# Kernel tuning notes

Measured on AMD Instinct MI355X. Metric: run time of the kernel, lower is better.

The kernel has to match this reference:

```python
import jax, jax.numpy as jnp
import numpy as np

W_SCALE = 0.1  # brevitas SignedBinaryWeightPerTensorConst default scaling_init
A_SCALE = 1.0  # brevitas SignedBinaryActPerTensorConst default scaling


def bin_weight(w):
    # fake-quant binary weight: scale * sign(w), STE identity gradient
    q = W_SCALE * jnp.sign(w)
    return w + jax.lax.stop_gradient(q - w)


def bin_act(x):
    # QuantHardTanh with signed binary act: clamp to [-1,1] then binarize (STE)
    y = jnp.clip(x, -A_SCALE, A_SCALE)
    q = A_SCALE * jnp.sign(y)
    return y + jax.lax.stop_gradient(q - y)


def conv1d(x, w, b, stride=1):
    # x: [N,C,L], w: [O,I,K]
    y = jax.lax.conv_general_dilated(x, w, (stride,), 'VALID',
                                     dimension_numbers=('NCH', 'OIH', 'NCH'))
    return y + b[None, :, None]


def maxpool4(x):
    return jax.lax.reduce_window(x, -jnp.inf, jax.lax.max,
                                 (1, 1, 4), (1, 1, 4), 'VALID')


def bn1d(x, s, o):
    # eval-mode BatchNorm folded to per-channel affine: scale s, bias o
    if x.ndim == 3:
        return x * s[None, :, None] + o[None, :, None]
    return x * s[None, :] + o[None, :]


def setup_inputs() -> dict:
    key = jax.random.key(0)
    ks = jax.random.split(key, 24)
    f = jax.random.normal
    inp = {
        'x': f(ks[0], (128, 1, 16000), jnp.float32),
        'w1': f(ks[1], (128, 1, 80), jnp.float32),
        'b1': f(ks[2], (128,), jnp.float32),
        'bn1_s': jax.random.uniform(ks[3], (128,), jnp.float32),
        'bn1_b': f(ks[4], (128,), jnp.float32),
        'w2': f(ks[5], (128, 128, 3), jnp.float32),
        'b2': f(ks[6], (128,), jnp.float32),
        'bn2_s': jax.random.uniform(ks[7], (128,), jnp.float32),
        'bn2_b': f(ks[8], (128,), jnp.float32),
        'w3': f(ks[9], (256, 128, 3), jnp.float32),
        'b3': f(ks[10], (256,), jnp.float32),
        'bn3_s': jax.random.uniform(ks[11], (256,), jnp.float32),
        'bn3_b': f(ks[12], (256,), jnp.float32),
        'w5': f(ks[13], (512, 256, 3), jnp.float32),
        'b5': f(ks[14], (512,), jnp.float32),
        'bn5_s': jax.random.uniform(ks[15], (512,), jnp.float32),
        'bn5_b': f(ks[16], (512,), jnp.float32),
        'w_emb': f(ks[17], (512, 512, 14), jnp.float32),
        'b_emb': f(ks[18], (512,), jnp.float32),
        'wfc1': f(ks[19], (256, 512), jnp.float32),
        'bnfc1_s': jax.random.uniform(ks[20], (256,), jnp.float32),
        'bnfc1_b': f(ks[21], (256,), jnp.float32),
        'wfc2': f(ks[22], (35, 256), jnp.float32),
    }
    return inp


def reference(x, w1, b1, bn1_s, bn1_b, w2, b2, bn2_s, bn2_b,
              w3, b3, bn3_s, bn3_b, w5, b5, bn5_s, bn5_b,
              w_emb, b_emb, wfc1, bnfc1_s, bnfc1_b, wfc2):
    x = conv1d(x, bin_weight(w1), b1, stride=4)      # [N,128,3981]
    x = maxpool4(bin_act(bn1d(x, bn1_s, bn1_b)))     # [N,128,995]
    x = conv1d(x, bin_weight(w2), b2)                # [N,128,993]
    x = maxpool4(bin_act(bn1d(x, bn2_s, bn2_b)))     # [N,128,248]
    x = conv1d(x, bin_weight(w3), b3)                # [N,256,246]
    x = maxpool4(bin_act(bn1d(x, bn3_s, bn3_b)))     # [N,256,61]
    x = conv1d(x, bin_weight(w5), b5)                # [N,512,59]
    x = maxpool4(bin_act(bn1d(x, bn5_s, bn5_b)))     # [N,512,14]
    x = conv1d(x, bin_weight(w_emb), b_emb)          # [N,512,1]
    x = x[:, :, 0]                                   # squeeze -> [N,512]
    x = x @ bin_weight(wfc1).T                       # [N,256]
    x = bin_act(bn1d(x, bnfc1_s, bnfc1_b))
    x = x @ bin_weight(wfc2).T                       # [N,35]
    return x
```

## Files before the change

### kernel.cpp

```cpp
#include <hip/hip_runtime.h>
#include <stdint.h>

__device__ __forceinline__ float dance(float w) {
  float q = w > 0.f ? 0.1f : (w < 0.f ? -0.1f : 0.0f);
  float r = __fsub_rn(q, w);
  return __fadd_rn(w, r);
}

__device__ __forceinline__ int sgn(float u) {
  return u > 0.f ? 1 : (u < 0.f ? -1 : 0);
}

__global__ void pack_dance_T(const float* __restrict__ w, float* __restrict__ out,
                             int OC, int K) {
  int idx = blockIdx.x * 256 + threadIdx.x;
  if (idx >= OC * K) return;
  int oc = idx / K, k = idx - oc * K;
  out[(size_t)k * OC + oc] = dance(w[idx]);
}

__global__ void pack_dance_W12(const float* __restrict__ w, float* __restrict__ out,
                               int OC, int K) {
  int idx = blockIdx.x * 256 + threadIdx.x;
  if (idx >= OC * K) return;
  int oc = idx / K, k = idx - oc * K;
  out[((size_t)(k / 12) * OC + oc) * 12 + (k % 12)] = dance(w[idx]);
}

__global__ void pack_dance_E4(const float* __restrict__ w, float* __restrict__ out,
                              int OC, int K) {
  int idx = blockIdx.x * 256 + threadIdx.x;
  if (idx >= OC * K) return;
  int r = idx >> 2;
  int lo = idx & 3;
  int oc = r % OC;
  int k4 = r / OC;
  out[idx] = dance(w[(size_t)oc * K + k4 * 4 + lo]);
}

__global__ __launch_bounds__(128) void conv1_fast(
    const float* __restrict__ x, const float* __restrict__ w1t,
    const float* __restrict__ b1, const float* __restrict__ s1,
    const float* __restrict__ o1, int8_t* __restrict__ a1) {
  const int tid = threadIdx.x;
  const int tp0 = blockIdx.x * 2;
  const int b0 = blockIdx.y * 2;
  float wreg[80];
#pragma unroll
  for (int k = 0; k < 80; ++k) wreg[k] = w1t[k * 128 + tid];

  const int sb0 = 4 * (min(tp0 + 0, 994) - tp0);
  const int sb1 = 4 * (min(tp0 + 1, 994) - tp0);
  const float4* xb0 = (const float4*)(x + (size_t)(b0 + 0) * 16000 + 16 * tp0);
  const float4* xb1 = (const float4*)(x + (size_t)(b0 + 1) * 16000 + 16 * tp0);
  float z[2][2][4] = {};
#pragma unroll
  for (int q = 0; q < 20; ++q) {
#pragma unroll
    for (int nb = 0; nb < 2; ++nb) {
      const float4* x4 = nb ? xb1 : xb0;
#pragma unroll
      for (int p = 0; p < 2; ++p) {
        const int sb = p ? sb1 : sb0;
        float4 v0 = x4[sb + q + 0];
        float4 v1 = x4[sb + q + 1];
        float4 v2 = x4[sb + q + 2];
        float4 v3 = x4[sb + q + 3];
        float4 vv[4] = {v0, v1, v2, v3};
#pragma unroll
        for (int g = 0; g < 4; ++g) {
          float zz = z[nb][p][g];
          zz = __builtin_fmaf(wreg[4 * q + 0], vv[g].x, zz);
          zz = __builtin_fmaf(wreg[4 * q + 1], vv[g].y, zz);
          zz = __builtin_fmaf(wreg[4 * q + 2], vv[g].z, zz);
          zz = __builtin_fmaf(wreg[4 * q + 3], vv[g].w, zz);
          z[nb][p][g] = zz;
        }
      }
    }
  }
  const float bv = b1[tid], sv = s1[tid], ov = o1[tid];
#pragma unroll
  for (int nb = 0; nb < 2; ++nb)
#pragma unroll
    for (int p = 0; p < 2; ++p) {
      int m = -2;
#pragma unroll
      for (int g = 0; g < 4; ++g) {
        float y = __fadd_rn(z[nb][p][g], bv);
        float t2 = __fmul_rn(y, sv);
        float u = __fadd_rn(t2, ov);
        m = max(m, sgn(u));
      }
      int tpc = min(tp0 + p, 994);
      a1[((size_t)(b0 + nb) * 995 + tpc) * 128 + tid] = (int8_t)m;
    }
}

template <int CIN, int COUT, int NOC, int TY, int NTP, int NB, bool OUTF>
__global__ __launch_bounds__((COUT / NOC) * TY) void convN_fast(
    const int8_t* __restrict__ ain, const float* __restrict__ wt,
    const float* __restrict__ bias, const float* __restrict__ bns,
    const float* __restrict__ bno, void* __restrict__ aout,
    int Tin, int TPout) {
  constexpr int LANES = COUT / NOC;
  constexpr int ROWS = 4 * TY * NTP + 2;
  constexpr int NT = LANES * TY;
  __shared__ __align__(16) float as_[NB][ROWS][CIN];
  const int tid = threadIdx.x;
  const int ocl = tid % LANES;
  const int ty = tid / LANES;
  const int tp0 = blockIdx.x * (TY * NTP);
  const int b0 = blockIdx.y * NB;
  for (int t = tid; t < NB * ROWS * CIN; t += NT) {
    int nb = t / (ROWS * CIN);
    int rem = t - nb * (ROWS * CIN);
    int r = rem / CIN, c = rem - r * CIN;
    int gr = min(4 * tp0 + r, Tin - 1);
    as_[nb][r][c] = (float)ain[((size_t)(b0 + nb) * Tin + gr) * CIN + c];
  }
  __syncthreads();

  float z[NOC][NB][NTP][4] = {};
#pragma unroll 2
  for (int i = 0; i < CIN; i += 4) {
    const int i4 = i >> 2;
    float wf[NOC][12];
#pragma unroll
    for (int j = 0; j < NOC; ++j) {
      const float* wp = wt + ((size_t)i4 * COUT + (ocl + j * LANES)) * 12;
      *(float4*)(wf[j] + 0) = *(const float4*)(wp + 0);
      *(float4*)(wf[j] + 4) = *(const float4*)(wp + 4);
      *(float4*)(wf[j] + 8) = *(const float4*)(wp + 8);
    }
#pragma unroll
    for (int nb = 0; nb < NB; ++nb)
#pragma unroll
      for (int p = 0; p < NTP; ++p) {
        const int rbase = 4 * (NTP * ty + p);
        float r6[6][4];
#pragma unroll
        for (int r = 0; r < 6; ++r)
          *(float4*)r6[r] = *(const float4*)&as_[nb][rbase + r][i];
#pragma unroll
        for (int j = 0; j < NOC; ++j)
#pragma unroll
          for (int g = 0; g < 4; ++g) {
            float zz = z[j][nb][p][g];
#pragma unroll
            for (int ii = 0; ii < 4; ++ii) {
              zz = __builtin_fmaf(wf[j][ii * 3 + 0], r6[g + 0][ii], zz);
              zz = __builtin_fmaf(wf[j][ii * 3 + 1], r6[g + 1][ii], zz);
              zz = __builtin_fmaf(wf[j][ii * 3 + 2], r6[g + 2][ii], zz);
            }
            z[j][nb][p][g] = zz;
          }
      }
  }
#pragma unroll
  for (int j = 0; j < NOC; ++j) {
    const int oc = ocl + j * LANES;
    const float bv = bias[oc], sv = bns[oc], ov = bno[oc];
#pragma unroll
    for (int nb = 0; nb < NB; ++nb)
#pragma unroll
      for (int p = 0; p < NTP; ++p) {
        const int tp = tp0 + NTP * ty + p;
        if (tp < TPout) {
          int m = -2;
#pragma unroll
          for (int g = 0; g < 4; ++g) {
            float y = __fadd_rn(z[j][nb][p][g], bv);
            float t2 = __fmul_rn(y, sv);
            float u = __fadd_rn(t2, ov);
            m = max(m, sgn(u));
          }
          if (OUTF)
            ((float*)aout)[(size_t)(b0 + nb) * (TPout * COUT) + (size_t)oc * TPout + tp] =
                (float)m;
          else
            ((int8_t*)aout)[((size_t)(b0 + nb) * TPout + tp) * COUT + oc] = (int8_t)m;
        }
      }
  }
}

__global__ __launch_bounds__(256) void emb_v5(
    const float* __restrict__ a4f, const float* __restrict__ wE4,
    const float* __restrict__ bemb, float* __restrict__ yemb) {
  __shared__ __align__(16) float av[7168];
  const int tid = threadIdx.x;
  const int oc = blockIdx.x * 256 + tid;
  const int b = blockIdx.y;
  const float* arow = a4f + (size_t)b * 7168;
  for (int i = tid * 4; i < 7168; i += 1024)
    *(float4*)&av[i] = *(const float4*)(arow + i);
  __syncthreads();
  const float4* wp = (const float4*)wE4 + oc;
  float z = 0.f;
#pragma unroll 8
  for (int k4 = 0; k4 < 1792; ++k4) {
    const float4 w4 = wp[(size_t)k4 * 512];
    const float4 v = *(const float4*)&av[k4 * 4];
    z = __builtin_fmaf(w4.x, v.x, z);
    z = __builtin_fmaf(w4.y, v.y, z);
    z = __builtin_fmaf(w4.z, v.z, z);
    z = __builtin_fmaf(w4.w, v.w, z);
  }
  yemb[(size_t)b * 512 + oc] = __fadd_rn(z, bemb[oc]);
}

__global__ __launch_bounds__(256) void fc_np(
    const float* __restrict__ yemb, const float* __restrict__ w1t,
    const float* __restrict__ s1, const float* __restrict__ o1,
    const float* __restrict__ w2t, float* __restrict__ out) {
  __shared__ float ys[512];
  __shared__ float a5[256];
  const int b = blockIdx.x;
  const int tid = threadIdx.x;
  for (int i = tid; i < 512; i += 256) ys[i] = yemb[(size_t)b * 512 + i];
  __syncthreads();
  float z = 0.f;
  for (int k = 0; k < 512; ++k)
    z = __builtin_fmaf(w1t[k * 256 + tid], ys[k], z);
  float t = __fmul_rn(z, s1[tid]);
  float u = __fadd_rn(t, o1[tid]);
  a5[tid] = u > 0.f ? 1.f : (u < 0.f ? -1.f : 0.f);
  __syncthreads();
  if (tid < 35) {
    float z2 = 0.f;
    for (int k = 0; k < 256; ++k)
      z2 = __builtin_fmaf(w2t[k * 35 + tid], a5[k], z2);
    out[(size_t)b * 35 + tid] = z2;
  }
}

extern "C" void kernel_launch(void* const* d_in, const int* in_sizes, int n_in,
                              void* d_out, int out_size, void* d_ws, size_t ws_size,
                              hipStream_t stream) {
  const float* x    = (const float*)d_in[0];
  const float* w1   = (const float*)d_in[1];
  const float* b1   = (const float*)d_in[2];
  const float* bn1s = (const float*)d_in[3];
  const float* bn1b = (const float*)d_in[4];
  const float* w2   = (const float*)d_in[5];
  const float* b2   = (const float*)d_in[6];
  const float* bn2s = (const float*)d_in[7];
  const float* bn2b = (const float*)d_in[8];
  const float* w3   = (const float*)d_in[9];
  const float* b3   = (const float*)d_in[10];
  const float* bn3s = (const float*)d_in[11];
  const float* bn3b = (const float*)d_in[12];
  const float* w5   = (const float*)d_in[13];
  const float* b5   = (const float*)d_in[14];
  const float* bn5s = (const float*)d_in[15];
  const float* bn5b = (const float*)d_in[16];
  const float* wemb = (const float*)d_in[17];
  const float* bemb = (const float*)d_in[18];
  const float* wfc1 = (const float*)d_in[19];
  const float* fc1s = (const float*)d_in[20];
  const float* fc1b = (const float*)d_in[21];
  const float* wfc2 = (const float*)d_in[22];
  float* out = (float*)d_out;

  uint8_t* ws = (uint8_t*)d_ws;
  size_t off = 0;
  auto carve = [&](size_t bytes) {
    void* p = ws + off;
    off = (off + bytes + 255) & ~(size_t)255;
    return p;
  };
  int8_t* a1   = (int8_t*)carve((size_t)128 * 995 * 128);
  int8_t* a2   = (int8_t*)carve((size_t)128 * 248 * 128);
  int8_t* a3   = (int8_t*)carve((size_t)128 * 61 * 256);
  float* a4f   = (float*)carve((size_t)128 * 512 * 14 * 4);
  float* yemb  = (float*)carve((size_t)128 * 512 * 4);
  float* w1t   = (float*)carve((size_t)80 * 128 * 4);
  float* wt2   = (float*)carve((size_t)384 * 128 * 4);
  float* wt3   = (float*)carve((size_t)384 * 256 * 4);
  float* wt5   = (float*)carve((size_t)768 * 512 * 4);
  float* wE4   = (float*)carve((size_t)7168 * 512 * 4);
  float* fc1t  = (float*)carve((size_t)512 * 256 * 4);
  float* fc2t  = (float*)carve((size_t)256 * 35 * 4);

  pack_dance_T<<<dim3((128 * 80 + 255) / 256), 256, 0, stream>>>(w1, w1t, 128, 80);
  pack_dance_W12<<<dim3((128 * 384 + 255) / 256), 256, 0, stream>>>(w2, wt2, 128, 384);
  pack_dance_W12<<<dim3((256 * 384 + 255) / 256), 256, 0, stream>>>(w3, wt3, 256, 384);
  pack_dance_W12<<<dim3((512 * 768 + 255) / 256), 256, 0, stream>>>(w5, wt5, 512, 768);
  pack_dance_E4<<<dim3((512 * 7168 + 255) / 256), 256, 0, stream>>>(wemb, wE4, 512, 7168);
  pack_dance_T<<<dim3((256 * 512 + 255) / 256), 256, 0, stream>>>(wfc1, fc1t, 256, 512);
  pack_dance_T<<<dim3((35 * 256 + 255) / 256), 256, 0, stream>>>(wfc2, fc2t, 35, 256);

  conv1_fast<<<dim3(498, 64), 128, 0, stream>>>(x, w1t, b1, bn1s, bn1b, a1);

  convN_fast<128, 128, 4, 2, 2, 1, false><<<dim3(62, 128), 64, 0, stream>>>(
      a1, wt2, b2, bn2s, bn2b, a2, 995, 248);
  convN_fast<128, 256, 4, 1, 2, 1, false><<<dim3(31, 128), 64, 0, stream>>>(
      a2, wt3, b3, bn3s, bn3b, a3, 248, 61);
  convN_fast<256, 512, 4, 1, 1, 1, true><<<dim3(14, 128), 128, 0, stream>>>(
      a3, wt5, b5, bn5s, bn5b, a4f, 61, 14);

  emb_v5<<<dim3(2, 128), 256, 0, stream>>>(a4f, wE4, bemb, yemb);

  fc_np<<<dim3(128), 256, 0, stream>>>(yemb, fc1t, fc1s, fc1b, fc2t, out);
}
```

Measured before the change: 709.1 us.

## Store activations as fp32 and read conv inputs directly from global memory

Intermediate activations change from int8 to float32, and the convolution kernels drop their shared-memory staging plus barrier, instead loading float4 rows straight from global (L2/L1-cached) memory. Layer-2 work is split across more blocks with fewer output channels per thread, and the activation buffers are aliased to save workspace. This removes the int8-to-float conversion, the LDS fill and the sync. In exchange it quadruples activation traffic and depends on caches to capture the reuse that shared memory provided before.

```diff
diff --git a/kernel.cpp b/kernel.cpp
--- a/kernel.cpp
+++ b/kernel.cpp
@@ -41,7 +41,7 @@
 __global__ __launch_bounds__(128) void conv1_fast(
     const float* __restrict__ x, const float* __restrict__ w1t,
     const float* __restrict__ b1, const float* __restrict__ s1,
-    const float* __restrict__ o1, int8_t* __restrict__ a1) {
+    const float* __restrict__ o1, float* __restrict__ a1f) {
   const int tid = threadIdx.x;
   const int tp0 = blockIdx.x * 2;
   const int b0 = blockIdx.y * 2;
@@ -93,35 +93,23 @@
         m = max(m, sgn(u));
       }
       int tpc = min(tp0 + p, 994);
-      a1[((size_t)(b0 + nb) * 995 + tpc) * 128 + tid] = (int8_t)m;
-    }
-}
-
-template <int CIN, int COUT, int NOC, int TY, int NTP, int NB, bool OUTF>
-__global__ __launch_bounds__((COUT / NOC) * TY) void convN_fast(
-    const int8_t* __restrict__ ain, const float* __restrict__ wt,
+      a1f[((size_t)(b0 + nb) * 995 + tpc) * 128 + tid] = (float)m;
+    }
+}
+
+template <int CIN, int COUT, int NOC, int NTP, bool OUTF>
+__global__ __launch_bounds__(COUT / NOC) void convS(
+    const float* __restrict__ ainf, const float* __restrict__ wt,
     const float* __restrict__ bias, const float* __restrict__ bns,
-    const float* __restrict__ bno, void* __restrict__ aout,
+    const float* __restrict__ bno, float* __restrict__ aout,
     int Tin, int TPout) {
   constexpr int LANES = COUT / NOC;
-  constexpr int ROWS = 4 * TY * NTP + 2;
-  constexpr int NT = LANES * TY;
-  __shared__ __align__(16) float as_[NB][ROWS][CIN];
-  const int tid = threadIdx.x;
-  const int ocl = tid % LANES;
-  const int ty = tid / LANES;
-  const int tp0 = blockIdx.x * (TY * NTP);
-  const int b0 = blockIdx.y * NB;
-  for (int t = tid; t < NB * ROWS * CIN; t += NT) {
-    int nb = t / (ROWS * CIN);
-    int rem = t - nb * (ROWS * CIN);
-    int r = rem / CIN, c = rem - r * CIN;
-    int gr = min(4 * tp0 + r, Tin - 1);
-    as_[nb][r][c] = (float)ain[((size_t)(b0 + nb) * Tin + gr) * CIN + c];
-  }
-  __syncthreads();
-
-  float z[NOC][NB][NTP][4] = {};
+  const int ocl = threadIdx.x;
+  const int tp0 = blockIdx.x * NTP;
+  const int b = blockIdx.y;
+  const float* arow = ainf + (size_t)b * Tin * CIN;
+
+  float z[NOC][NTP][4] = {};
 #pragma unroll 2
   for (int i = 0; i < CIN; i += 4) {
     const int i4 = i >> 2;
@@ -134,54 +122,50 @@
       *(float4*)(wf[j] + 8) = *(const float4*)(wp + 8);
     }
 #pragma unroll
-    for (int nb = 0; nb < NB; ++nb)
-#pragma unroll
-      for (int p = 0; p < NTP; ++p) {
-        const int rbase = 4 * (NTP * ty + p);
-        float r6[6][4];
-#pragma unroll
-        for (int r = 0; r < 6; ++r)
-          *(float4*)r6[r] = *(const float4*)&as_[nb][rbase + r][i];
-#pragma unroll
-        for (int j = 0; j < NOC; ++j)
-#pragma unroll
-          for (int g = 0; g < 4; ++g) {
-            float zz = z[j][nb][p][g];
-#pragma unroll
-            for (int ii = 0; ii < 4; ++ii) {
-              zz = __builtin_fmaf(wf[j][ii * 3 + 0], r6[g + 0][ii], zz);
-              zz = __builtin_fmaf(wf[j][ii * 3 + 1], r6[g + 1][ii], zz);
-              zz = __builtin_fmaf(wf[j][ii * 3 + 2], r6[g + 2][ii], zz);
-            }
-            z[j][nb][p][g] = zz;
+    for (int p = 0; p < NTP; ++p) {
+      float r6[6][4];
+#pragma unroll
+      for (int r = 0; r < 6; ++r) {
+        const int gr = min(4 * tp0 + 4 * p + r, Tin - 1);
+        *(float4*)r6[r] = *(const float4*)&arow[(size_t)gr * CIN + i];
+      }
+#pragma unroll
+      for (int j = 0; j < NOC; ++j)
+#pragma unroll
+        for (int g = 0; g < 4; ++g) {
+          float zz = z[j][p][g];
+#pragma unroll
+          for (int ii = 0; ii < 4; ++ii) {
+            zz = __builtin_fmaf(wf[j][ii * 3 + 0], r6[g + 0][ii], zz);
+            zz = __builtin_fmaf(wf[j][ii * 3 + 1], r6[g + 1][ii], zz);
+            zz = __builtin_fmaf(wf[j][ii * 3 + 2], r6[g + 2][ii], zz);
           }
-      }
+          z[j][p][g] = zz;
+        }
+    }
   }
 #pragma unroll
   for (int j = 0; j < NOC; ++j) {
     const int oc = ocl + j * LANES;
     const float bv = bias[oc], sv = bns[oc], ov = bno[oc];
 #pragma unroll
-    for (int nb = 0; nb < NB; ++nb)
-#pragma unroll
-      for (int p = 0; p < NTP; ++p) {
-        const int tp = tp0 + NTP * ty + p;
-        if (tp < TPout) {
-          int m = -2;
-#pragma unroll
-          for (int g = 0; g < 4; ++g) {
-            float y = __fadd_rn(z[j][nb][p][g], bv);
-            float t2 = __fmul_rn(y, sv);
-            float u = __fadd_rn(t2, ov);
-            m = max(m, sgn(u));
-          }
-          if (OUTF)
-            ((float*)aout)[(size_t)(b0 + nb) * (TPout * COUT) + (size_t)oc * TPout + tp] =
-                (float)m;
-          else
-            ((int8_t*)aout)[((size_t)(b0 + nb) * TPout + tp) * COUT + oc] = (int8_t)m;
+    for (int p = 0; p < NTP; ++p) {
+      const int tp = tp0 + p;
+      if (tp < TPout) {
+        int m = -2;
+#pragma unroll
+        for (int g = 0; g < 4; ++g) {
+          float y = __fadd_rn(z[j][p][g], bv);
+          float t2 = __fmul_rn(y, sv);
+          float u = __fadd_rn(t2, ov);
+          m = max(m, sgn(u));
         }
-      }
+        if (OUTF)
+          aout[(size_t)b * (TPout * COUT) + (size_t)oc * TPout + tp] = (float)m;
+        else
+          aout[((size_t)b * TPout + tp) * COUT + oc] = (float)m;
+      }
+    }
   }
 }
 
@@ -270,10 +254,10 @@
     off = (off + bytes + 255) & ~(size_t)255;
     return p;
   };
-  int8_t* a1   = (int8_t*)carve((size_t)128 * 995 * 128);
-  int8_t* a2   = (int8_t*)carve((size_t)128 * 248 * 128);
-  int8_t* a3   = (int8_t*)carve((size_t)128 * 61 * 256);
-  float* a4f   = (float*)carve((size_t)128 * 512 * 14 * 4);
+  float* a1f   = (float*)carve((size_t)128 * 995 * 128 * 4);
+  float* a3f   = a1f;
+  float* a4f   = a1f + (size_t)128 * 61 * 256 + 64;
+  float* a2f   = (float*)carve((size_t)128 * 248 * 128 * 4);
   float* yemb  = (float*)carve((size_t)128 * 512 * 4);
   float* w1t   = (float*)carve((size_t)80 * 128 * 4);
   float* wt2   = (float*)carve((size_t)384 * 128 * 4);
@@ -291,14 +275,14 @@
   pack_dance_T<<<dim3((256 * 512 + 255) / 256), 256, 0, stream>>>(wfc1, fc1t, 256, 512);
   pack_dance_T<<<dim3((35 * 256 + 255) / 256), 256, 0, stream>>>(wfc2, fc2t, 35, 256);
 
-  conv1_fast<<<dim3(498, 64), 128, 0, stream>>>(x, w1t, b1, bn1s, bn1b, a1);
-
-  convN_fast<128, 128, 4, 2, 2, 1, false><<<dim3(62, 128), 64, 0, stream>>>(
-      a1, wt2, b2, bn2s, bn2b, a2, 995, 248);
-  convN_fast<128, 256, 4, 1, 2, 1, false><<<dim3(31, 128), 64, 0, stream>>>(
-      a2, wt3, b3, bn3s, bn3b, a3, 248, 61);
-  convN_fast<256, 512, 4, 1, 1, 1, true><<<dim3(14, 128), 128, 0, stream>>>(
-      a3, wt5, b5, bn5s, bn5b, a4f, 61, 14);
+  conv1_fast<<<dim3(498, 64), 128, 0, stream>>>(x, w1t, b1, bn1s, bn1b, a1f);
+
+  convS<128, 128, 2, 2, false><<<dim3(124, 128), 64, 0, stream>>>(
+      a1f, wt2, b2, bn2s, bn2b, a2f, 995, 248);
+  convS<128, 256, 4, 2, false><<<dim3(31, 128), 64, 0, stream>>>(
+      a2f, wt3, b3, bn3s, bn3b, a3f, 248, 61);
+  convS<256, 512, 4, 1, true><<<dim3(14, 128), 128, 0, stream>>>(
+      a3f, wt5, b5, bn5s, bn5b, a4f, 61, 14);
 
   emb_v5<<<dim3(2, 128), 256, 0, stream>>>(a4f, wE4, bemb, yemb);
 
```

Result: no change. 716.0 us (+1.0%).
